# Kernel tuning notes

Hardware: AMD Instinct MI355X
Metric: run time of the kernel (lower is better)

## Reference

```python
import jax, jax.numpy as jnp
import numpy as np
from jax import lax

N_TAPS = 27  # 3x3x3 kernel

def _gather_one(xb, ti, hi, wi):
    # xb: (C,T,H,W); ti/hi/wi: (T,H,W) int32. Zero-fill outside bounds.
    C, T, H, W = xb.shape
    valid = (ti >= 0) & (ti < T) & (hi >= 0) & (hi < H) & (wi >= 0) & (wi < W)
    lin = (jnp.clip(ti, 0, T - 1) * H + jnp.clip(hi, 0, H - 1)) * W + jnp.clip(wi, 0, W - 1)
    v = jnp.take(xb.reshape(C, -1), lin.reshape(-1), axis=1).reshape(C, T, H, W)
    return v * valid.astype(xb.dtype)

_gather = jax.vmap(_gather_one)  # over batch

def _trilinear(x, t, h, w):
    # x: (B,C,T,H,W); t/h/w: (B,T,H,W) float sample coordinates.
    t0, h0, w0 = jnp.floor(t), jnp.floor(h), jnp.floor(w)
    lt, lh, lw = t - t0, h - h0, w - w0
    t0i, h0i, w0i = t0.astype(jnp.int32), h0.astype(jnp.int32), w0.astype(jnp.int32)
    acc = 0.0
    for ti, wt in ((t0i, 1.0 - lt), (t0i + 1, lt)):
        for hi, wh in ((h0i, 1.0 - lh), (h0i + 1, lh)):
            for wi, ww in ((w0i, 1.0 - lw), (w0i + 1, lw)):
                acc = acc + _gather(x, ti, hi, wi) * (wt * wh * ww)[:, None]
    return acc  # (B,C,T,H,W)

def _deform_conv3d(x, offset_w, offset_b, weight):
    # x: (B,Cin,T,H,W). Offset layout: (B, 3, 27, T, H, W), axis1=(dt,dh,dw),
    # tap index k = kt*9 + kh*3 + kw. stride=1, padding=1, dilation=1, no bias.
    off = lax.conv_general_dilated(
        x, offset_w, (1, 1, 1), [(1, 1)] * 3,
        dimension_numbers=("NCDHW", "OIDHW", "NCDHW"))
    off = off + offset_b[None, :, None, None, None]
    B, _, T, H, W = off.shape
    off = off.reshape(B, 3, N_TAPS, T, H, W)
    tg = jnp.arange(T, dtype=x.dtype)[:, None, None]
    hg = jnp.arange(H, dtype=x.dtype)[None, :, None]
    wg = jnp.arange(W, dtype=x.dtype)[None, None, :]
    out = jnp.zeros((B, weight.shape[0], T, H, W), x.dtype)
    for k in range(N_TAPS):
        kt, kh, kw = k // 9, (k // 3) % 3, k % 3
        t = tg + (kt - 1) + off[:, 0, k]
        h = hg + (kh - 1) + off[:, 1, k]
        w = wg + (kw - 1) + off[:, 2, k]
        s = _trilinear(x, t, h, w)  # (B,Cin,T,H,W)
        out = out + jnp.einsum('bcthw,oc->bothw', s, weight[:, :, kt, kh, kw])
    return out

def setup_inputs() -> dict:
    key = jax.random.key(0)
    ks = jax.random.split(key, 4)
    B, T, C, H, W = 1, 4, 64, 128, 128
    x = jax.random.normal(ks[0], (B, T, C, H, W), jnp.float32)
    # small init scale keeps predicted offsets in a realistic +-2px range
    offset_w = jax.random.normal(ks[1], (3 * N_TAPS, C, 3, 3, 3), jnp.float32) * 0.02
    offset_b = jnp.zeros((3 * N_TAPS,), jnp.float32)
    weight = jax.random.normal(ks[2], (C, C, 3, 3, 3), jnp.float32) * 0.02
    gamma = jax.random.normal(ks[3], (1,), jnp.float32) * 0.1
    return {"x": x, "offset_w": offset_w, "offset_b": offset_b,
            "weight": weight, "gamma": gamma}

def reference(x, offset_w, offset_b, weight, gamma):
    xp = jnp.transpose(x, (0, 2, 1, 3, 4))  # (B,C,T,H,W)
    xc = _deform_conv3d(xp, offset_w, offset_b, weight)
    return gamma[0] * jnp.transpose(xc, (0, 2, 1, 3, 4)) + x
```

## Files before the change

### kernel.cpp

```cpp
#include <hip/hip_runtime.h>
#include <cmath>

#define Cc 64
#define Hh 128
#define Ww 128
#define HW_ 16384
#define THW_ 65536
#define CHW_ 1048576
#define NT 27

typedef unsigned short ushort_t;
typedef _Float16 f16x2 __attribute__((ext_vector_type(2)));
typedef _Float16 f16x8 __attribute__((ext_vector_type(8)));
typedef __fp16 fp16x2_alt __attribute__((ext_vector_type(2)));
typedef float floatx4 __attribute__((ext_vector_type(4)));
typedef unsigned uint4v __attribute__((ext_vector_type(4)));

union U32H2 { unsigned u; f16x2 h; };

static __device__ inline ushort_t f2h(float f) {
  union { _Float16 h; ushort_t u; } v;
  v.h = (_Float16)f;
  return v.u;
}

static __device__ inline unsigned pk2(float a) {
  union { fp16x2_alt h; unsigned u; } v;
  v.h = __builtin_amdgcn_cvt_pkrtz(a, a);
  return v.u;
}

#if defined(__has_builtin)
#if __has_builtin(__builtin_amdgcn_make_buffer_rsrc) && __has_builtin(__builtin_amdgcn_raw_buffer_load_b32) && __has_builtin(__builtin_amdgcn_raw_buffer_load_b128)
#define USE_BUF 1
#endif
#endif
#ifndef USE_BUF
#define USE_BUF 0
#endif

struct XtBuf {
#if USE_BUF
  __amdgpu_buffer_rsrc_t r;
#else
  const char* p;
#endif
};

static __device__ inline XtBuf mkbuf(const ushort_t* xt) {
  XtBuf b;
#if USE_BUF
  b.r = __builtin_amdgcn_make_buffer_rsrc((void*)xt, (short)0, 8388608, 0x00020000);
#else
  b.p = (const char*)xt;
#endif
  return b;
}

static __device__ inline uint4v xload4(const XtBuf& b, unsigned voff) {
#if USE_BUF
  return __builtin_amdgcn_raw_buffer_load_b128(b.r, (int)voff, 0, 0);
#else
  return *(const uint4v*)(b.p + voff);
#endif
}


__global__ __launch_bounds__(256) void prep(
    const float* __restrict__ offset_w,
    const float* __restrict__ weight,
    ushort_t* __restrict__ w2frag,
    ushort_t* __restrict__ wfrag)
{
  int e = blockIdx.x * 256 + threadIdx.x;
  if (e < 165888) {
    int j = e & 7, ln = (e >> 3) & 63, kh2 = (e >> 9) & 1, r = e >> 10;
    int ot = r % 6, k = r / 6;
    int oc = ot * 16 + (ln & 15);
    int c  = kh2 * 32 + (ln >> 4) * 8 + j;
    float v = (oc < 81) ? offset_w[(oc * 64 + c) * 27 + k] : 0.f;
    w2frag[e] = f2h(v);
  }
  if (e < 110592) {
    int j = e & 7, ln = (e >> 3) & 63, kh2 = (e >> 9) & 1, r = e >> 10;
    int ot = r & 3, k = r >> 2;
    int o = ot * 16 + (ln & 15);
    int c = kh2 * 32 + (ln >> 4) * 8 + j;
    wfrag[e] = f2h(weight[(o * 64 + c) * 27 + k]);
  }
}

__global__ __launch_bounds__(256) void transpose_x(
    const float* __restrict__ x, ushort_t* __restrict__ xt)
{
  __shared__ float tile[64][65];
  int b = blockIdx.x;
  int wblk = b & 1;
  int th = b >> 1;
  int h = th & 127;
  int t = th >> 7;
  int w0 = wblk * 64;
  int lane = threadIdx.x & 63;
  int quad = threadIdx.x >> 6;
  #pragma unroll
  for (int cc = 0; cc < 16; ++cc) {
    int c = cc * 4 + quad;
    tile[c][lane] = x[t * CHW_ + c * HW_ + h * Ww + w0 + lane];
  }
  __syncthreads();
  #pragma unroll
  for (int ww = 0; ww < 16; ++ww) {
    int w = ww * 4 + quad;
    xt[(size_t)(t * HW_ + h * Ww + w0 + w) * 64 + lane] = f2h(tile[lane][w]);
  }
}

#define SITE(W, D, A0, A1, A2, A3) \
  { U32H2 wu; wu.u = (W); U32H2 q0, q1, q2, q3; \
    q0.u = (D)[0]; q1.u = (D)[1]; q2.u = (D)[2]; q3.u = (D)[3]; \
    A0 += wu.h * q0.h; A1 += wu.h * q1.h; A2 += wu.h * q2.h; A3 += wu.h * q3.h; }

__global__ __launch_bounds__(256, 4) void fused(
    const float* __restrict__ x,
    const ushort_t* __restrict__ xt,
    const ushort_t* __restrict__ w2frag,
    const float* __restrict__ ob,
    const ushort_t* __restrict__ wfrag,
    const float* __restrict__ gamma,
    float* __restrict__ out)
{
  __shared__ __align__(16) char lds[38480];
  ushort_t* S = (ushort_t*)lds;
  unsigned* msite0 = (unsigned*)(lds + 9216);
  unsigned* msite1 = (unsigned*)(lds + 11264);
  unsigned* mwt0   = (unsigned*)(lds + 13312);
  unsigned* mwt1   = (unsigned*)(lds + 15360);
  float* Obuf = (float*)(lds + 17408);
  float* Dbuf = (float*)lds;
  int lane = threadIdx.x & 63;
  int wavei = __builtin_amdgcn_readfirstlane(threadIdx.x >> 6);
  int quad = lane >> 4;
  int m16 = lane & 15;
  int g8 = lane >> 3;
  unsigned coff = (unsigned)((lane & 7) * 16);
  int bid0 = blockIdx.x;
  int p0 = ((bid0 & 7) * 128 + (bid0 >> 3)) * 64;
  int t = p0 >> 14;
  int h = (p0 >> 7) & 127;
  int w0 = p0 & 127;
  XtBuf xb = mkbuf(xt);

  {
    floatx4 acc[6];
    #pragma unroll
    for (int i = 0; i < 6; ++i) acc[i] = (floatx4){0.f, 0.f, 0.f, 0.f};

    uint4v pd[2];

    auto issue = [&](int k) {
      int kt = k / 9, kh = (k / 3) % 3, kw = k % 3;
      int ts = t + kt - 1, hs = h + kh - 1;
      int tsc = min(max(ts, 0), 3);
      int hsc = min(max(hs, 0), 127);
      int sbase = tsc * HW_ + hsc * Ww;
      #pragma unroll
      for (int b = 0; b < 2; ++b) {
        int prow = wavei * 16 + b * 8 + g8;
        int wc = w0 + prow + kw - 1;
        int wcc = min(max(wc, 0), 127);
        pd[b] = xload4(xb, ((unsigned)(sbase + wcc) << 7) + coff);
      }
    };

    issue(0);
    #pragma unroll 1
    for (int k = 0; k < NT; ++k) {
      int kt = k / 9, kh = (k / 3) % 3, kw = k % 3;
      int ts = t + kt - 1, hs = h + kh - 1;
      bool rowok = ((unsigned)ts < 4u) && ((unsigned)hs < 128u);
      #pragma unroll
      for (int b = 0; b < 2; ++b) {
        int prow = wavei * 16 + b * 8 + g8;
        int wc = w0 + prow + kw - 1;
        bool ok = rowok && ((unsigned)wc < 128u);
        uint4v v = pd[b];
        if (!ok) v = (uint4v){0u, 0u, 0u, 0u};
        *(uint4v*)((char*)S + prow * 144 + coff) = v;
      }
      if (k + 1 < NT) issue(k + 1);
      const ushort_t* srow = S + (wavei * 16 + m16) * 72 + quad * 8;
      f16x8 af0 = *(const f16x8*)srow;
      f16x8 af1 = *(const f16x8*)(srow + 32);
      #pragma unroll
      for (int ot = 0; ot < 6; ++ot) {
        const ushort_t* wb = w2frag + (size_t)((k * 6 + ot) * 2) * 512 + lane * 8;
        f16x8 b0 = *(const f16x8*)(wb);
        f16x8 b1 = *(const f16x8*)(wb + 512);
        acc[ot] = __builtin_amdgcn_mfma_f32_16x16x32_f16(af0, b0, acc[ot], 0, 0, 0);
        acc[ot] = __builtin_amdgcn_mfma_f32_16x16x32_f16(af1, b1, acc[ot], 0, 0, 0);
      }
    }
    #pragma unroll
    for (int ot = 0; ot < 6; ++ot) {
      int oc = ot * 16 + m16;
      if (oc < 81) {
        float bv = ob[oc];
        #pragma unroll
        for (int r = 0; r < 4; ++r)
          Obuf[oc * 65 + wavei * 16 + quad * 4 + r] = acc[ot][r] + bv;
      }
    }
  }

  floatx4 acc[4];
  #pragma unroll
  for (int i = 0; i < 4; ++i) acc[i] = (floatx4){0.f, 0.f, 0.f, 0.f};

  int pl = wavei * 16 + m16;
  int aq = quad >> 1, bq = quad & 1;
  int rowA = wavei * 16 + g8;
  int rowB = rowA + 8;

  uint4v stA[8], stB[8];

  auto meta = [&](int kk, float dtv, float dhv, float dwv) {
    unsigned* ms = (kk & 1) ? msite1 : msite0;
    unsigned* mw = (kk & 1) ? mwt1 : mwt0;
    int kt = kk / 9, kh = (kk / 3) % 3, kw = kk % 3;
    float tf = (float)(t + kt - 1) + dtv;
    float hf = (float)(h + kh - 1) + dhv;
    float wf = (float)(w0 + pl + kw - 1) + dwv;
    float tF = floorf(tf), hF = floorf(hf), wF = floorf(wf);
    float lt = tf - tF, lh_ = hf - hF, lw_ = wf - wF;
    int t0 = (int)tF, h0 = (int)hF, wq_ = (int)wF;
    int ti = t0 + aq;
    float wt_ = (aq ? lt : 1.f - lt) * (((unsigned)ti < 4u) ? 1.f : 0.f);
    int tic = min(max(ti, 0), 3);
    int hi = h0 + bq;
    float wh_ = (bq ? lh_ : 1.f - lh_) * (((unsigned)hi < 128u) ? 1.f : 0.f);
    int hic = min(max(hi, 0), 127);
    int base2 = tic * HW_ + hic * Ww;
    float bw = wt_ * wh_;
    int wi0 = wq_;
    float ww0 = (1.f - lw_) * (((unsigned)wi0 < 128u) ? 1.f : 0.f);
    int wi0c = min(max(wi0, 0), 127);
    int wi1 = wq_ + 1;
    float ww1 = lw_ * (((unsigned)wi1 < 128u) ? 1.f : 0.f);
    int wi1c = min(max(wi1, 0), 127);
    uint2 sp_;
    sp_.x = (unsigned)(base2 + wi0c) << 7;
    sp_.y = (unsigned)(base2 + wi1c) << 7;
    *(uint2*)&ms[pl * 8 + quad * 2] = sp_;
    uint2 wp_;
    wp_.x = pk2(bw * ww0);
    wp_.y = pk2(bw * ww1);
    *(uint2*)&mw[pl * 8 + quad * 2] = wp_;
  };

  auto issueA = [&](int kk) {
    const unsigned* ms = (kk & 1) ? msite1 : msite0;
    const uint4* sp = (const uint4*)&ms[rowA * 8];
    uint4 s0 = sp[0], s1 = sp[1];
    stA[0] = xload4(xb, s0.x + coff);
    stA[1] = xload4(xb, s0.y + coff);
    stA[2] = xload4(xb, s0.z + coff);
    stA[3] = xload4(xb, s0.w + coff);
    stA[4] = xload4(xb, s1.x + coff);
    stA[5] = xload4(xb, s1.y + coff);
    stA[6] = xload4(xb, s1.z + coff);
    stA[7] = xload4(xb, s1.w + coff);
  };
  auto issueB = [&](int kk) {
    const unsigned* ms = (kk & 1) ? msite1 : msite0;
    const uint4* sp = (const uint4*)&ms[rowB * 8];
    uint4 s0 = sp[0], s1 = sp[1];
    stB[0] = xload4(xb, s0.x + coff);
    stB[1] = xload4(xb, s0.y + coff);
    stB[2] = xload4(xb, s0.z + coff);
    stB[3] = xload4(xb, s0.w + coff);
    stB[4] = xload4(xb, s1.x + coff);
    stB[5] = xload4(xb, s1.y + coff);
    stB[6] = xload4(xb, s1.z + coff);
    stB[7] = xload4(xb, s1.w + coff);
  };

  auto consumeA = [&](int kk) {
    const unsigned* mw = (kk & 1) ? mwt1 : mwt0;
    const uint4* wp = (const uint4*)&mw[rowA * 8];
    uint4 w03 = wp[0], w47 = wp[1];
    U32H2 z; z.u = 0;
    f16x2 e0 = z.h, e1 = z.h, e2 = z.h, e3 = z.h;
    f16x2 o0 = z.h, o1 = z.h, o2 = z.h, o3 = z.h;
    SITE(w03.x, stA[0], e0, e1, e2, e3)
    SITE(w03.y, stA[1], o0, o1, o2, o3)
    SITE(w03.z, stA[2], e0, e1, e2, e3)
    SITE(w03.w, stA[3], o0, o1, o2, o3)
    SITE(w47.x, stA[4], e0, e1, e2, e3)
    SITE(w47.y, stA[5], o0, o1, o2, o3)
    SITE(w47.z, stA[6], e0, e1, e2, e3)
    SITE(w47.w, stA[7], o0, o1, o2, o3)
    U32H2 r0, r1, r2, r3;
    r0.h = e0 + o0; r1.h = e1 + o1; r2.h = e2 + o2; r3.h = e3 + o3;
    uint4v res = {r0.u, r1.u, r2.u, r3.u};
    *(uint4v*)((char*)S + rowA * 144 + coff) = res;
  };
  auto consumeB = [&](int kk) {
    const unsigned* mw = (kk & 1) ? mwt1 : mwt0;
    const uint4* wp = (const uint4*)&mw[rowB * 8];
    uint4 w03 = wp[0], w47 = wp[1];
    U32H2 z; z.u = 0;
    f16x2 e0 = z.h, e1 = z.h, e2 = z.h, e3 = z.h;
    f16x2 o0 = z.h, o1 = z.h, o2 = z.h, o3 = z.h;
    SITE(w03.x, stB[0], e0, e1, e2, e3)
    SITE(w03.y, stB[1], o0, o1, o2, o3)
    SITE(w03.z, stB[2], e0, e1, e2, e3)
    SITE(w03.w, stB[3], o0, o1, o2, o3)
    SITE(w47.x, stB[4], e0, e1, e2, e3)
    SITE(w47.y, stB[5], o0, o1, o2, o3)
    SITE(w47.z, stB[6], e0, e1, e2, e3)
    SITE(w47.w, stB[7], o0, o1, o2, o3)
    U32H2 r0, r1, r2, r3;
    r0.h = e0 + o0; r1.h = e1 + o1; r2.h = e2 + o2; r3.h = e3 + o3;
    uint4v res = {r0.u, r1.u, r2.u, r3.u};
    *(uint4v*)((char*)S + rowB * 144 + coff) = res;
  };

  {
    float dt0 = Obuf[(0 * NT + 0) * 65 + pl];
    float dh0 = Obuf[(1 * NT + 0) * 65 + pl];
    float dw0 = Obuf[(2 * NT + 0) * 65 + pl];
    meta(0, dt0, dh0, dw0);
  }
  issueA(0);

  #pragma unroll 1
  for (int k = 0; k < NT; ++k) {
    int kn = (k + 1 < NT) ? k + 1 : NT - 1;
    float dt_n = Obuf[(0 * NT + kn) * 65 + pl];
    float dh_n = Obuf[(1 * NT + kn) * 65 + pl];
    float dw_n = Obuf[(2 * NT + kn) * 65 + pl];

    issueB(k);
    __builtin_amdgcn_sched_barrier(0);
    consumeA(k);
    if (k + 1 < NT) meta(kn, dt_n, dh_n, dw_n);
    consumeB(k);
    if (k + 1 < NT) issueA(kn);
    __builtin_amdgcn_sched_barrier(0);

    const ushort_t* srow = S + (wavei * 16 + m16) * 72 + quad * 8;
    f16x8 af0 = *(const f16x8*)srow;
    f16x8 af1 = *(const f16x8*)(srow + 32);
    #pragma unroll
    for (int ot = 0; ot < 4; ++ot) {
      const ushort_t* wb = wfrag + (size_t)((k * 4 + ot) * 2) * 512 + lane * 8;
      f16x8 b0 = *(const f16x8*)(wb);
      f16x8 b1 = *(const f16x8*)(wb + 512);
      acc[ot] = __builtin_amdgcn_mfma_f32_16x16x32_f16(af0, b0, acc[ot], 0, 0, 0);
      acc[ot] = __builtin_amdgcn_mfma_f32_16x16x32_f16(af1, b1, acc[ot], 0, 0, 0);
    }
  }
  __syncthreads();
  #pragma unroll
  for (int ot = 0; ot < 4; ++ot)
    #pragma unroll
    for (int r = 0; r < 4; ++r)
      Dbuf[(ot * 16 + m16) * 65 + wavei * 16 + quad * 4 + r] = acc[ot][r];
  __syncthreads();
  float g = gamma[0];
  for (int i = threadIdx.x; i < 64 * 64; i += 256) {
    int oc = i >> 6, p = i & 63;
    size_t oi = (size_t)t * CHW_ + (size_t)oc * HW_ + (size_t)h * Ww + w0 + p;
    out[oi] = fmaf(g, Dbuf[oc * 65 + p], x[oi]);
  }
}

extern "C" void kernel_launch(void* const* d_in, const int* in_sizes, int n_in,
                              void* d_out, int out_size, void* d_ws, size_t ws_size,
                              hipStream_t stream) {
  (void)in_sizes; (void)n_in; (void)out_size; (void)ws_size;
  const float* x        = (const float*)d_in[0];
  const float* offset_w = (const float*)d_in[1];
  const float* offset_b = (const float*)d_in[2];
  const float* weight   = (const float*)d_in[3];
  const float* gamma    = (const float*)d_in[4];
  float* out = (float*)d_out;
  float* wsf = (float*)d_ws;
  ushort_t* xt     = (ushort_t*)(wsf + 5308416);
  ushort_t* wfrag  = (ushort_t*)(wsf + 7405568);
  ushort_t* w2frag = (ushort_t*)(wsf + 7460864);

  hipLaunchKernelGGL(prep, dim3(648), dim3(256), 0, stream,
                     offset_w, weight, w2frag, wfrag);
  hipLaunchKernelGGL(transpose_x, dim3(1024), dim3(256), 0, stream, x, xt);
  hipLaunchKernelGGL(fused, dim3(1024), dim3(256), 0, stream,
                     x, xt, w2frag, offset_b, wfrag, gamma, out);
}
```

Before: 208.1 us.

## Shrink fused blocks to 32 pixels, pack site metadata, merge prep kernels

Merges the weight prep and x-transpose kernels into one launch, which removes a kernel launch. The fused kernel now uses 128-thread blocks covering 32 pixels, twice as many blocks, and a much smaller LDS footprint, so more blocks can be resident per CU. Site offsets and fp16 bilinear weights are packed into one 32-bit word in a single LDS metadata buffer, and the weight is broadcast with a byte permute. This drops the double-buffered meta arrays, but consumers must now read metadata the same iteration it is written, which relies on per-wave ordering. The packed offset field is limited to 16 bits, which still covers the 65536 sites in x.

```diff
diff --git a/kernel.cpp b/kernel.cpp
--- a/kernel.cpp
+++ b/kernel.cpp
@@ -30,6 +30,18 @@
   return v.u;
 }
 
+static __device__ inline unsigned rep16(unsigned p) {
+#if defined(__has_builtin)
+#if __has_builtin(__builtin_amdgcn_perm)
+  return __builtin_amdgcn_perm(p, p, 0x01000100u);
+#else
+  return (p & 0xFFFFu) * 0x10001u;
+#endif
+#else
+  return (p & 0xFFFFu) * 0x10001u;
+#endif
+}
+
 #if defined(__has_builtin)
 #if __has_builtin(__builtin_amdgcn_make_buffer_rsrc) && __has_builtin(__builtin_amdgcn_raw_buffer_load_b32) && __has_builtin(__builtin_amdgcn_raw_buffer_load_b128)
 #define USE_BUF 1
@@ -66,52 +78,51 @@
 }
 
 
-__global__ __launch_bounds__(256) void prep(
+__global__ __launch_bounds__(256) void prep_transpose(
+    const float* __restrict__ x, ushort_t* __restrict__ xt,
     const float* __restrict__ offset_w,
     const float* __restrict__ weight,
     ushort_t* __restrict__ w2frag,
     ushort_t* __restrict__ wfrag)
 {
-  int e = blockIdx.x * 256 + threadIdx.x;
-  if (e < 165888) {
-    int j = e & 7, ln = (e >> 3) & 63, kh2 = (e >> 9) & 1, r = e >> 10;
-    int ot = r % 6, k = r / 6;
-    int oc = ot * 16 + (ln & 15);
-    int c  = kh2 * 32 + (ln >> 4) * 8 + j;
-    float v = (oc < 81) ? offset_w[(oc * 64 + c) * 27 + k] : 0.f;
-    w2frag[e] = f2h(v);
-  }
-  if (e < 110592) {
-    int j = e & 7, ln = (e >> 3) & 63, kh2 = (e >> 9) & 1, r = e >> 10;
-    int ot = r & 3, k = r >> 2;
-    int o = ot * 16 + (ln & 15);
-    int c = kh2 * 32 + (ln >> 4) * 8 + j;
-    wfrag[e] = f2h(weight[(o * 64 + c) * 27 + k]);
-  }
-}
-
-__global__ __launch_bounds__(256) void transpose_x(
-    const float* __restrict__ x, ushort_t* __restrict__ xt)
-{
   __shared__ float tile[64][65];
-  int b = blockIdx.x;
-  int wblk = b & 1;
-  int th = b >> 1;
-  int h = th & 127;
-  int t = th >> 7;
-  int w0 = wblk * 64;
-  int lane = threadIdx.x & 63;
-  int quad = threadIdx.x >> 6;
-  #pragma unroll
-  for (int cc = 0; cc < 16; ++cc) {
-    int c = cc * 4 + quad;
-    tile[c][lane] = x[t * CHW_ + c * HW_ + h * Ww + w0 + lane];
-  }
-  __syncthreads();
-  #pragma unroll
-  for (int ww = 0; ww < 16; ++ww) {
-    int w = ww * 4 + quad;
-    xt[(size_t)(t * HW_ + h * Ww + w0 + w) * 64 + lane] = f2h(tile[lane][w]);
+  if (blockIdx.x < 1024) {
+    int b = blockIdx.x;
+    int wblk = b & 1;
+    int th = b >> 1;
+    int h = th & 127;
+    int t = th >> 7;
+    int w0 = wblk * 64;
+    int lane = threadIdx.x & 63;
+    int quad = threadIdx.x >> 6;
+    #pragma unroll
+    for (int cc = 0; cc < 16; ++cc) {
+      int c = cc * 4 + quad;
+      tile[c][lane] = x[t * CHW_ + c * HW_ + h * Ww + w0 + lane];
+    }
+    __syncthreads();
+    #pragma unroll
+    for (int ww = 0; ww < 16; ++ww) {
+      int w = ww * 4 + quad;
+      xt[(size_t)(t * HW_ + h * Ww + w0 + w) * 64 + lane] = f2h(tile[lane][w]);
+    }
+  } else {
+    int e = (blockIdx.x - 1024) * 256 + threadIdx.x;
+    if (e < 165888) {
+      int j = e & 7, ln = (e >> 3) & 63, kh2 = (e >> 9) & 1, r = e >> 10;
+      int ot = r % 6, k = r / 6;
+      int oc = ot * 16 + (ln & 15);
+      int c  = kh2 * 32 + (ln >> 4) * 8 + j;
+      float v = (oc < 81) ? offset_w[(oc * 64 + c) * 27 + k] : 0.f;
+      w2frag[e] = f2h(v);
+    }
+    if (e < 110592) {
+      int j = e & 7, ln = (e >> 3) & 63, kh2 = (e >> 9) & 1, r = e >> 10;
+      int ot = r & 3, k = r >> 2;
+      int o = ot * 16 + (ln & 15);
+      int c = kh2 * 32 + (ln >> 4) * 8 + j;
+      wfrag[e] = f2h(weight[(o * 64 + c) * 27 + k]);
+    }
   }
 }
 
@@ -120,7 +131,7 @@
     q0.u = (D)[0]; q1.u = (D)[1]; q2.u = (D)[2]; q3.u = (D)[3]; \
     A0 += wu.h * q0.h; A1 += wu.h * q1.h; A2 += wu.h * q2.h; A3 += wu.h * q3.h; }
 
-__global__ __launch_bounds__(256, 4) void fused(
+__global__ __launch_bounds__(128, 5) void fused(
     const float* __restrict__ x,
     const ushort_t* __restrict__ xt,
     const ushort_t* __restrict__ w2frag,
@@ -129,13 +140,10 @@
     const float* __restrict__ gamma,
     float* __restrict__ out)
 {
-  __shared__ __align__(16) char lds[38480];
+  __shared__ __align__(16) char lds[16324];
   ushort_t* S = (ushort_t*)lds;
-  unsigned* msite0 = (unsigned*)(lds + 9216);
-  unsigned* msite1 = (unsigned*)(lds + 11264);
-  unsigned* mwt0   = (unsigned*)(lds + 13312);
-  unsigned* mwt1   = (unsigned*)(lds + 15360);
-  float* Obuf = (float*)(lds + 17408);
+  unsigned* pmeta = (unsigned*)(lds + 4608);
+  float* Obuf = (float*)(lds + 5632);
   float* Dbuf = (float*)lds;
   int lane = threadIdx.x & 63;
   int wavei = __builtin_amdgcn_readfirstlane(threadIdx.x >> 6);
@@ -144,7 +152,7 @@
   int g8 = lane >> 3;
   unsigned coff = (unsigned)((lane & 7) * 16);
   int bid0 = blockIdx.x;
-  int p0 = ((bid0 & 7) * 128 + (bid0 >> 3)) * 64;
+  int p0 = ((bid0 & 7) * 256 + (bid0 >> 3)) * 32;
   int t = p0 >> 14;
   int h = (p0 >> 7) & 127;
   int w0 = p0 & 127;
@@ -207,7 +215,7 @@
         float bv = ob[oc];
         #pragma unroll
         for (int r = 0; r < 4; ++r)
-          Obuf[oc * 65 + wavei * 16 + quad * 4 + r] = acc[ot][r] + bv;
+          Obuf[oc * 33 + wavei * 16 + quad * 4 + r] = acc[ot][r] + bv;
       }
     }
   }
@@ -222,10 +230,9 @@
   int rowB = rowA + 8;
 
   uint4v stA[8], stB[8];
+  uint4 pmA0, pmA1, pmB0, pmB1;
 
   auto meta = [&](int kk, float dtv, float dhv, float dwv) {
-    unsigned* ms = (kk & 1) ? msite1 : msite0;
-    unsigned* mw = (kk & 1) ? mwt1 : mwt0;
     int kt = kk / 9, kh = (kk / 3) % 3, kw = kk % 3;
     float tf = (float)(t + kt - 1) + dtv;
     float hf = (float)(h + kh - 1) + dhv;
@@ -247,78 +254,73 @@
     int wi1 = wq_ + 1;
     float ww1 = lw_ * (((unsigned)wi1 < 128u) ? 1.f : 0.f);
     int wi1c = min(max(wi1, 0), 127);
-    uint2 sp_;
-    sp_.x = (unsigned)(base2 + wi0c) << 7;
-    sp_.y = (unsigned)(base2 + wi1c) << 7;
-    *(uint2*)&ms[pl * 8 + quad * 2] = sp_;
-    uint2 wp_;
-    wp_.x = pk2(bw * ww0);
-    wp_.y = pk2(bw * ww1);
-    *(uint2*)&mw[pl * 8 + quad * 2] = wp_;
-  };
-
-  auto issueA = [&](int kk) {
-    const unsigned* ms = (kk & 1) ? msite1 : msite0;
-    const uint4* sp = (const uint4*)&ms[rowA * 8];
-    uint4 s0 = sp[0], s1 = sp[1];
-    stA[0] = xload4(xb, s0.x + coff);
-    stA[1] = xload4(xb, s0.y + coff);
-    stA[2] = xload4(xb, s0.z + coff);
-    stA[3] = xload4(xb, s0.w + coff);
-    stA[4] = xload4(xb, s1.x + coff);
-    stA[5] = xload4(xb, s1.y + coff);
-    stA[6] = xload4(xb, s1.z + coff);
-    stA[7] = xload4(xb, s1.w + coff);
-  };
-  auto issueB = [&](int kk) {
-    const unsigned* ms = (kk & 1) ? msite1 : msite0;
-    const uint4* sp = (const uint4*)&ms[rowB * 8];
-    uint4 s0 = sp[0], s1 = sp[1];
-    stB[0] = xload4(xb, s0.x + coff);
-    stB[1] = xload4(xb, s0.y + coff);
-    stB[2] = xload4(xb, s0.z + coff);
-    stB[3] = xload4(xb, s0.w + coff);
-    stB[4] = xload4(xb, s1.x + coff);
-    stB[5] = xload4(xb, s1.y + coff);
-    stB[6] = xload4(xb, s1.z + coff);
-    stB[7] = xload4(xb, s1.w + coff);
-  };
-
-  auto consumeA = [&](int kk) {
-    const unsigned* mw = (kk & 1) ? mwt1 : mwt0;
-    const uint4* wp = (const uint4*)&mw[rowA * 8];
-    uint4 w03 = wp[0], w47 = wp[1];
+    uint2 mp_;
+    mp_.x = ((unsigned)(base2 + wi0c) << 16) | (pk2(bw * ww0) & 0xFFFFu);
+    mp_.y = ((unsigned)(base2 + wi1c) << 16) | (pk2(bw * ww1) & 0xFFFFu);
+    *(uint2*)&pmeta[pl * 8 + quad * 2] = mp_;
+  };
+
+  auto mread = [&]() {
+    const uint4* mpA = (const uint4*)&pmeta[rowA * 8];
+    pmA0 = mpA[0]; pmA1 = mpA[1];
+    const uint4* mpB = (const uint4*)&pmeta[rowB * 8];
+    pmB0 = mpB[0]; pmB1 = mpB[1];
+  };
+
+  auto vof = [&](unsigned p) -> unsigned {
+    return ((p >> 9) & 0xFFFFFF80u) + coff;
+  };
+
+  auto issueA = [&]() {
+    stA[0] = xload4(xb, vof(pmA0.x));
+    stA[1] = xload4(xb, vof(pmA0.y));
+    stA[2] = xload4(xb, vof(pmA0.z));
+    stA[3] = xload4(xb, vof(pmA0.w));
+    stA[4] = xload4(xb, vof(pmA1.x));
+    stA[5] = xload4(xb, vof(pmA1.y));
+    stA[6] = xload4(xb, vof(pmA1.z));
+    stA[7] = xload4(xb, vof(pmA1.w));
+  };
+  auto issueB = [&]() {
+    stB[0] = xload4(xb, vof(pmB0.x));
+    stB[1] = xload4(xb, vof(pmB0.y));
+    stB[2] = xload4(xb, vof(pmB0.z));
+    stB[3] = xload4(xb, vof(pmB0.w));
+    stB[4] = xload4(xb, vof(pmB1.x));
+    stB[5] = xload4(xb, vof(pmB1.y));
+    stB[6] = xload4(xb, vof(pmB1.z));
+    stB[7] = xload4(xb, vof(pmB1.w));
+  };
+
+  auto consumeA = [&]() {
     U32H2 z; z.u = 0;
     f16x2 e0 = z.h, e1 = z.h, e2 = z.h, e3 = z.h;
     f16x2 o0 = z.h, o1 = z.h, o2 = z.h, o3 = z.h;
-    SITE(w03.x, stA[0], e0, e1, e2, e3)
-    SITE(w03.y, stA[1], o0, o1, o2, o3)
-    SITE(w03.z, stA[2], e0, e1, e2, e3)
-    SITE(w03.w, stA[3], o0, o1, o2, o3)
-    SITE(w47.x, stA[4], e0, e1, e2, e3)
-    SITE(w47.y, stA[5], o0, o1, o2, o3)
-    SITE(w47.z, stA[6], e0, e1, e2, e3)
-    SITE(w47.w, stA[7], o0, o1, o2, o3)
+    SITE(rep16(pmA0.x), stA[0], e0, e1, e2, e3)
+    SITE(rep16(pmA0.y), stA[1], o0, o1, o2, o3)
+    SITE(rep16(pmA0.z), stA[2], e0, e1, e2, e3)
+    SITE(rep16(pmA0.w), stA[3], o0, o1, o2, o3)
+    SITE(rep16(pmA1.x), stA[4], e0, e1, e2, e3)
+    SITE(rep16(pmA1.y), stA[5], o0, o1, o2, o3)
+    SITE(rep16(pmA1.z), stA[6], e0, e1, e2, e3)
+    SITE(rep16(pmA1.w), stA[7], o0, o1, o2, o3)
     U32H2 r0, r1, r2, r3;
     r0.h = e0 + o0; r1.h = e1 + o1; r2.h = e2 + o2; r3.h = e3 + o3;
     uint4v res = {r0.u, r1.u, r2.u, r3.u};
     *(uint4v*)((char*)S + rowA * 144 + coff) = res;
   };
-  auto consumeB = [&](int kk) {
-    const unsigned* mw = (kk & 1) ? mwt1 : mwt0;
-    const uint4* wp = (const uint4*)&mw[rowB * 8];
-    uint4 w03 = wp[0], w47 = wp[1];
+  auto consumeB = [&]() {
     U32H2 z; z.u = 0;
     f16x2 e0 = z.h, e1 = z.h, e2 = z.h, e3 = z.h;
     f16x2 o0 = z.h, o1 = z.h, o2 = z.h, o3 = z.h;
-    SITE(w03.x, stB[0], e0, e1, e2, e3)
-    SITE(w03.y, stB[1], o0, o1, o2, o3)
-    SITE(w03.z, stB[2], e0, e1, e2, e3)
-    SITE(w03.w, stB[3], o0, o1, o2, o3)
-    SITE(w47.x, stB[4], e0, e1, e2, e3)
-    SITE(w47.y, stB[5], o0, o1, o2, o3)
-    SITE(w47.z, stB[6], e0, e1, e2, e3)
-    SITE(w47.w, stB[7], o0, o1, o2, o3)
+    SITE(rep16(pmB0.x), stB[0], e0, e1, e2, e3)
+    SITE(rep16(pmB0.y), stB[1], o0, o1, o2, o3)
+    SITE(rep16(pmB0.z), stB[2], e0, e1, e2, e3)
+    SITE(rep16(pmB0.w), stB[3], o0, o1, o2, o3)
+    SITE(rep16(pmB1.x), stB[4], e0, e1, e2, e3)
+    SITE(rep16(pmB1.y), stB[5], o0, o1, o2, o3)
+    SITE(rep16(pmB1.z), stB[6], e0, e1, e2, e3)
+    SITE(rep16(pmB1.w), stB[7], o0, o1, o2, o3)
     U32H2 r0, r1, r2, r3;
     r0.h = e0 + o0; r1.h = e1 + o1; r2.h = e2 + o2; r3.h = e3 + o3;
     uint4v res = {r0.u, r1.u, r2.u, r3.u};
@@ -326,26 +328,27 @@
   };
 
   {
-    float dt0 = Obuf[(0 * NT + 0) * 65 + pl];
-    float dh0 = Obuf[(1 * NT + 0) * 65 + pl];
-    float dw0 = Obuf[(2 * NT + 0) * 65 + pl];
+    float dt0 = Obuf[(0 * NT + 0) * 33 + pl];
+    float dh0 = Obuf[(1 * NT + 0) * 33 + pl];
+    float dw0 = Obuf[(2 * NT + 0) * 33 + pl];
     meta(0, dt0, dh0, dw0);
   }
-  issueA(0);
+  mread();
+  issueA();
 
   #pragma unroll 1
   for (int k = 0; k < NT; ++k) {
     int kn = (k + 1 < NT) ? k + 1 : NT - 1;
-    float dt_n = Obuf[(0 * NT + kn) * 65 + pl];
-    float dh_n = Obuf[(1 * NT + kn) * 65 + pl];
-    float dw_n = Obuf[(2 * NT + kn) * 65 + pl];
-
-    issueB(k);
+    float dt_n = Obuf[(0 * NT + kn) * 33 + pl];
+    float dh_n = Obuf[(1 * NT + kn) * 33 + pl];
+    float dw_n = Obuf[(2 * NT + kn) * 33 + pl];
+
+    issueB();
     __builtin_amdgcn_sched_barrier(0);
-    consumeA(k);
+    consumeA();
     if (k + 1 < NT) meta(kn, dt_n, dh_n, dw_n);
-    consumeB(k);
-    if (k + 1 < NT) issueA(kn);
+    consumeB();
+    if (k + 1 < NT) { mread(); issueA(); }
     __builtin_amdgcn_sched_barrier(0);
 
     const ushort_t* srow = S + (wavei * 16 + m16) * 72 + quad * 8;
@@ -365,13 +368,13 @@
   for (int ot = 0; ot < 4; ++ot)
     #pragma unroll
     for (int r = 0; r < 4; ++r)
-      Dbuf[(ot * 16 + m16) * 65 + wavei * 16 + quad * 4 + r] = acc[ot][r];
+      Dbuf[(ot * 16 + m16) * 33 + wavei * 16 + quad * 4 + r] = acc[ot][r];
   __syncthreads();
   float g = gamma[0];
-  for (int i = threadIdx.x; i < 64 * 64; i += 256) {
-    int oc = i >> 6, p = i & 63;
+  for (int i = threadIdx.x; i < 64 * 32; i += 128) {
+    int oc = i >> 5, p = i & 31;
     size_t oi = (size_t)t * CHW_ + (size_t)oc * HW_ + (size_t)h * Ww + w0 + p;
-    out[oi] = fmaf(g, Dbuf[oc * 65 + p], x[oi]);
+    out[oi] = fmaf(g, Dbuf[oc * 33 + p], x[oi]);
   }
 }
 
@@ -390,9 +393,8 @@
   ushort_t* wfrag  = (ushort_t*)(wsf + 7405568);
   ushort_t* w2frag = (ushort_t*)(wsf + 7460864);
 
-  hipLaunchKernelGGL(prep, dim3(648), dim3(256), 0, stream,
-                     offset_w, weight, w2frag, wfrag);
-  hipLaunchKernelGGL(transpose_x, dim3(1024), dim3(256), 0, stream, x, xt);
-  hipLaunchKernelGGL(fused, dim3(1024), dim3(256), 0, stream,
+  hipLaunchKernelGGL(prep_transpose, dim3(1672), dim3(256), 0, stream,
+                     x, xt, offset_w, weight, w2frag, wfrag);
+  hipLaunchKernelGGL(fused, dim3(2048), dim3(128), 0, stream,
                      x, xt, w2frag, offset_b, wfrag, gamma, out);
 }
```

After: 395.3 us. 89.9% more time.
